# Kernel tuning notes

Hardware: AMD Instinct MI355X
Metric: run time of the kernel (lower is better)

## Reference

```python
import jax, jax.numpy as jnp
import numpy as np

B, S, NH, H, NKEYS = 2, 2048, 8, 64, 64


def setup_inputs() -> dict:
    key = jax.random.key(0)
    k1, k2, k3, k4 = jax.random.split(key, 4)
    q = jax.random.normal(k1, (B, S, NH, H), dtype=jnp.float32)
    k = jax.random.normal(k2, (B, S, NH, H), dtype=jnp.float32)
    v = jax.random.normal(k3, (B, S, NH, H), dtype=jnp.float32)
    # per-(batch, query) random key indices: randint(0, s1, (b, s2, n))
    indices = jax.random.randint(k4, (B, S, NKEYS), 0, S, dtype=jnp.int32)
    return {"q": q, "k": k, "v": v, "indices": indices}


def reference(q, k, v, indices):
    # q,k,v: (B, S, NH, H); indices: (B, S, n)
    b, s, nh, h = q.shape
    scale = h ** -0.5
    bi = jnp.arange(b)[:, None, None]  # (b,1,1) batch indexer
    kg = k[bi, indices]  # (b, s, n, nh, h) gathered keys
    vg = v[bi, indices]  # (b, s, n, nh, h) gathered values
    # A: (b, q, k, heads) == einsum('b q n h, b q k n h -> b q k n')
    A = jnp.einsum('bqeh,bqkeh->bqke', q * scale, kg)
    A = jax.nn.softmax(A, axis=-2)  # softmax over the n random keys (dim=-2)
    # dropout p=0 (eval) -> identity
    z = jnp.einsum('bqke,bqkeh->bqeh', A, vg)
    return z
```

## Files before the change

kernel.cpp:

```cpp
#include <hip/hip_runtime.h>


#define BB 2
#define SS 2048
#define NHH 8
#define HH 64
#define NKEYS 64

__global__ __launch_bounds__(256, 6) void rand_attn_kernel(
    const float* __restrict__ q, const float* __restrict__ k,
    const float* __restrict__ v, const int* __restrict__ idx,
    float* __restrict__ out) {
  const int tid = threadIdx.x;
  const int lane = tid & 63;
  const int g = lane >> 4;
  const int c = lane & 15;

  const int w = __builtin_amdgcn_readfirstlane(blockIdx.x * 4 + (tid >> 6));
  const int e = w & (NHH - 1);
  const int bq = w >> 3;
  const int b = bq >> 11;

  const float* kb = k + ((size_t)b * (SS * NHH * HH));
  const float* vb = v + ((size_t)b * (SS * NHH * HH));

  const int sco = e * (HH * 4) + c * 16;

  float4 q4 = ((const float4*)(q + ((size_t)bq * NHH + e) * HH))[c];
  const float qs = 0.125f * 1.44269504f;
  q4.x *= qs; q4.y *= qs; q4.z *= qs; q4.w *= qs;

  const int myidx = idx[bq * NKEYS + lane];

  float ssum = 0.f;
  float4 acc = make_float4(0.f, 0.f, 0.f, 0.f);
#pragma unroll
  for (int j = 0; j < 16; ++j) {
    const int vi = __builtin_amdgcn_ds_bpermute((4 * j + g) << 2, myidx);
    const int voff = (vi << 11) + sco;
    const float4 kv = *(const float4*)((const char*)kb + voff);
    const float4 vv = *(const float4*)((const char*)vb + voff);
    float t = kv.x * q4.x + kv.y * q4.y + kv.z * q4.z + kv.w * q4.w;
    t += __shfl_xor(t, 1, 64);
    t += __shfl_xor(t, 2, 64);
    t += __shfl_xor(t, 4, 64);
    t += __shfl_xor(t, 8, 64);
    const float p = __builtin_amdgcn_exp2f(t);
    ssum += p;
    acc.x += p * vv.x;
    acc.y += p * vv.y;
    acc.z += p * vv.z;
    acc.w += p * vv.w;
  }

  ssum += __shfl_xor(ssum, 16, 64);
  ssum += __shfl_xor(ssum, 32, 64);
  acc.x += __shfl_xor(acc.x, 16, 64);
  acc.y += __shfl_xor(acc.y, 16, 64);
  acc.z += __shfl_xor(acc.z, 16, 64);
  acc.w += __shfl_xor(acc.w, 16, 64);
  acc.x += __shfl_xor(acc.x, 32, 64);
  acc.y += __shfl_xor(acc.y, 32, 64);
  acc.z += __shfl_xor(acc.z, 32, 64);
  acc.w += __shfl_xor(acc.w, 32, 64);

  const float inv = 1.0f / ssum;
  acc.x *= inv; acc.y *= inv; acc.z *= inv; acc.w *= inv;

  if (g == 0) {
    *(float4*)((char*)(out + (size_t)w * HH) + c * 16) = acc;
  }
}

extern "C" void kernel_launch(void* const* d_in, const int* in_sizes, int n_in,
                              void* d_out, int out_size, void* d_ws,
                              size_t ws_size, hipStream_t stream) {
  const float* q = (const float*)d_in[0];
  const float* k = (const float*)d_in[1];
  const float* v = (const float*)d_in[2];
  const int* idx = (const int*)d_in[3];
  float* out = (float*)d_out;

  const int n_blocks = (BB * SS * NHH) / 4;
  rand_attn_kernel<<<n_blocks, 256, 0, stream>>>(q, k, v, idx, out);
}
```

Before: 117.5 us.

## Pack K and V into interleaved fp16 workspace before gathered attention

Adds a pre-pass kernel that converts K and V to fp16 and interleaves each row's K and V halves into one 256-byte record in workspace. The attention kernel then gathers a single 16-byte load per lane covering 8 K or 8 V values, swapping the score with a partner lane via shuffle. This halves gathered bytes and merges K/V fetches. It adds a full extra read/write pass over K and V every call, and fp16 rounding lowers precision.

```diff
diff --git a/kernel.cpp b/kernel.cpp
--- a/kernel.cpp
+++ b/kernel.cpp
@@ -1,4 +1,5 @@
 #include <hip/hip_runtime.h>
+#include <hip/hip_fp16.h>
 
 
 #define BB 2
@@ -7,68 +8,98 @@
 #define HH 64
 #define NKEYS 64
 
+__global__ __launch_bounds__(256) void pack_kv(
+    const float* __restrict__ k, const float* __restrict__ v,
+    __half* __restrict__ ws) {
+  const int t = blockIdx.x * 256 + threadIdx.x;
+  const int blk = t >> 4;
+  const int half = (t >> 3) & 1;
+  const int h8 = t & 7;
+  const float* src = (half ? v : k) + (size_t)blk * 64 + h8 * 8;
+  const float4 a = ((const float4*)src)[0];
+  const float4 b = ((const float4*)src)[1];
+  __half2 p0 = __floats2half2_rn(a.x, a.y);
+  __half2 p1 = __floats2half2_rn(a.z, a.w);
+  __half2 p2 = __floats2half2_rn(b.x, b.y);
+  __half2 p3 = __floats2half2_rn(b.z, b.w);
+  int4 o;
+  o.x = *(const int*)&p0; o.y = *(const int*)&p1;
+  o.z = *(const int*)&p2; o.w = *(const int*)&p3;
+  ((int4*)ws)[t] = o;
+}
+
 __global__ __launch_bounds__(256, 6) void rand_attn_kernel(
-    const float* __restrict__ q, const float* __restrict__ k,
-    const float* __restrict__ v, const int* __restrict__ idx,
-    float* __restrict__ out) {
+    const float* __restrict__ q, const int* __restrict__ idx,
+    const __half* __restrict__ kv, float* __restrict__ out) {
   const int tid = threadIdx.x;
   const int lane = tid & 63;
   const int g = lane >> 4;
-  const int c = lane & 15;
+  const int sub = lane & 15;
+  const int c8 = lane & 7;
 
   const int w = __builtin_amdgcn_readfirstlane(blockIdx.x * 4 + (tid >> 6));
   const int e = w & (NHH - 1);
   const int bq = w >> 3;
   const int b = bq >> 11;
 
-  const float* kb = k + ((size_t)b * (SS * NHH * HH));
-  const float* vb = v + ((size_t)b * (SS * NHH * HH));
+  const char* kvb = (const char*)kv + (size_t)b * (SS * NHH * 256);
+  const int sco = e * 256 + sub * 16;
 
-  const int sco = e * (HH * 4) + c * 16;
-
-  float4 q4 = ((const float4*)(q + ((size_t)bq * NHH + e) * HH))[c];
+  const float* qrow = q + (((size_t)bq * NHH + e) * HH) + c8 * 8;
+  float4 qa = ((const float4*)qrow)[0];
+  float4 qb = ((const float4*)qrow)[1];
   const float qs = 0.125f * 1.44269504f;
-  q4.x *= qs; q4.y *= qs; q4.z *= qs; q4.w *= qs;
+  qa.x *= qs; qa.y *= qs; qa.z *= qs; qa.w *= qs;
+  qb.x *= qs; qb.y *= qs; qb.z *= qs; qb.w *= qs;
 
   const int myidx = idx[bq * NKEYS + lane];
 
   float ssum = 0.f;
-  float4 acc = make_float4(0.f, 0.f, 0.f, 0.f);
+  float a0 = 0.f, a1 = 0.f, a2 = 0.f, a3 = 0.f;
+  float a4 = 0.f, a5 = 0.f, a6 = 0.f, a7 = 0.f;
+
 #pragma unroll
   for (int j = 0; j < 16; ++j) {
     const int vi = __builtin_amdgcn_ds_bpermute((4 * j + g) << 2, myidx);
     const int voff = (vi << 11) + sco;
-    const float4 kv = *(const float4*)((const char*)kb + voff);
-    const float4 vv = *(const float4*)((const char*)vb + voff);
-    float t = kv.x * q4.x + kv.y * q4.y + kv.z * q4.z + kv.w * q4.w;
+    const int4 raw = *(const int4*)(kvb + voff);
+    const float2 f0 = __half22float2(*(const __half2*)&raw.x);
+    const float2 f1 = __half22float2(*(const __half2*)&raw.y);
+    const float2 f2 = __half22float2(*(const __half2*)&raw.z);
+    const float2 f3 = __half22float2(*(const __half2*)&raw.w);
+    float t = f0.x * qa.x + f0.y * qa.y + f1.x * qa.z + f1.y * qa.w +
+              f2.x * qb.x + f2.y * qb.y + f3.x * qb.z + f3.y * qb.w;
     t += __shfl_xor(t, 1, 64);
     t += __shfl_xor(t, 2, 64);
     t += __shfl_xor(t, 4, 64);
-    t += __shfl_xor(t, 8, 64);
     const float p = __builtin_amdgcn_exp2f(t);
-    ssum += p;
-    acc.x += p * vv.x;
-    acc.y += p * vv.y;
-    acc.z += p * vv.z;
-    acc.w += p * vv.w;
+    const float pv = __shfl_xor(p, 8, 64);
+    ssum += pv;
+    a0 += pv * f0.x; a1 += pv * f0.y;
+    a2 += pv * f1.x; a3 += pv * f1.y;
+    a4 += pv * f2.x; a5 += pv * f2.y;
+    a6 += pv * f3.x; a7 += pv * f3.y;
   }
 
   ssum += __shfl_xor(ssum, 16, 64);
   ssum += __shfl_xor(ssum, 32, 64);
-  acc.x += __shfl_xor(acc.x, 16, 64);
-  acc.y += __shfl_xor(acc.y, 16, 64);
-  acc.z += __shfl_xor(acc.z, 16, 64);
-  acc.w += __shfl_xor(acc.w, 16, 64);
-  acc.x += __shfl_xor(acc.x, 32, 64);
-  acc.y += __shfl_xor(acc.y, 32, 64);
-  acc.z += __shfl_xor(acc.z, 32, 64);
-  acc.w += __shfl_xor(acc.w, 32, 64);
+  a0 += __shfl_xor(a0, 16, 64); a0 += __shfl_xor(a0, 32, 64);
+  a1 += __shfl_xor(a1, 16, 64); a1 += __shfl_xor(a1, 32, 64);
+  a2 += __shfl_xor(a2, 16, 64); a2 += __shfl_xor(a2, 32, 64);
+  a3 += __shfl_xor(a3, 16, 64); a3 += __shfl_xor(a3, 32, 64);
+  a4 += __shfl_xor(a4, 16, 64); a4 += __shfl_xor(a4, 32, 64);
+  a5 += __shfl_xor(a5, 16, 64); a5 += __shfl_xor(a5, 32, 64);
+  a6 += __shfl_xor(a6, 16, 64); a6 += __shfl_xor(a6, 32, 64);
+  a7 += __shfl_xor(a7, 16, 64); a7 += __shfl_xor(a7, 32, 64);
 
   const float inv = 1.0f / ssum;
-  acc.x *= inv; acc.y *= inv; acc.z *= inv; acc.w *= inv;
 
-  if (g == 0) {
-    *(float4*)((char*)(out + (size_t)w * HH) + c * 16) = acc;
+  if (g == 0 && sub >= 8) {
+    float* o = out + (size_t)w * HH + c8 * 8;
+    float4 lo = make_float4(a0 * inv, a1 * inv, a2 * inv, a3 * inv);
+    float4 hi = make_float4(a4 * inv, a5 * inv, a6 * inv, a7 * inv);
+    ((float4*)o)[0] = lo;
+    ((float4*)o)[1] = hi;
   }
 }
 
@@ -80,7 +111,8 @@
   const float* v = (const float*)d_in[2];
   const int* idx = (const int*)d_in[3];
   float* out = (float*)d_out;
+  __half* kv = (__half*)d_ws;
 
-  const int n_blocks = (BB * SS * NHH) / 4;
-  rand_attn_kernel<<<n_blocks, 256, 0, stream>>>(q, k, v, idx, out);
+  pack_kv<<<2048, 256, 0, stream>>>(k, v, kv);
+  rand_attn_kernel<<<(BB * SS * NHH) / 4, 256, 0, stream>>>(q, idx, kv, out);
 }
```

New measurement: 359.3 us. +205.9%, slower.
